# Performance work log

Hardware: AMD Instinct MI355X
Metric: run time of the kernel (lower is better)

Reference implementation:

```python
import jax, jax.numpy as jnp
import numpy as np

D_MODEL = 1024
N_HEAD = 16
HEAD_DIM = D_MODEL // N_HEAD

def setup_inputs() -> dict:
    key = jax.random.key(0)
    k1, k2, k3 = jax.random.split(key, 3)
    x = jax.random.normal(k1, (2, 2048, D_MODEL), dtype=jnp.float32)
    # torch Linear weights: [out_features, in_features]; scale like default init
    w_in = jax.random.normal(k2, (3 * D_MODEL, D_MODEL), dtype=jnp.float32) * (1.0 / np.sqrt(D_MODEL))
    w_out = jax.random.normal(k3, (D_MODEL, D_MODEL), dtype=jnp.float32) * (1.0 / np.sqrt(D_MODEL))
    return {"x": x, "w_in": w_in, "w_out": w_out}

def reference(x, w_in, w_out):
    B, T, D = x.shape
    qkv = jnp.einsum('btd,ed->bte', x, w_in)  # [B,T,3D]
    q, k, v = jnp.split(qkv, 3, axis=2)
    def heads(t):
        return t.reshape(B, T, N_HEAD, HEAD_DIM).transpose(0, 2, 1, 3)  # [B,H,T,hd]
    q, k, v = heads(q), heads(k), heads(v)
    att = jnp.einsum('bhqd,bhkd->bhqk', q, k) / np.sqrt(HEAD_DIM).astype(np.float32)
    # NOTE: original uses .tril() (zeroing, NOT -inf) before softmax — faithful reproduction
    causal = jnp.tril(jnp.ones((T, T), dtype=bool))
    att = jnp.where(causal, att, 0.0)
    att = jax.nn.softmax(att, axis=-1)
    out = jnp.einsum('bhqk,bhkd->bhqd', att, v)
    out = out.transpose(0, 2, 1, 3).reshape(B, T, D)
    return jnp.einsum('btd,ed->bte', out, w_out)
```

## Files before the change

### kernel.cpp

```cpp
#include <hip/hip_runtime.h>
#include <hip/hip_bf16.h>
#include <stdint.h>

#define TSEQ   2048
#define DMODEL 1024
#define NHEAD  16
#define HDIM   64

typedef __attribute__((ext_vector_type(8))) __bf16 bf16x8;
typedef __attribute__((ext_vector_type(4))) float f32x4;
typedef __attribute__((ext_vector_type(8))) unsigned short u16x8;

#define SC_LOG2E 0.18033688011112042f

#if __has_builtin(__builtin_amdgcn_exp2f)
#define EXP2F(x) __builtin_amdgcn_exp2f(x)
#else
#define EXP2F(x) __expf(0.6931471805599453f * (x))
#endif

__device__ __forceinline__ unsigned short f2bf(float f) {
    __hip_bfloat16 h = __float2bfloat16(f);
    return __builtin_bit_cast(unsigned short, h);
}
__device__ __forceinline__ float bf2f(unsigned short u) {
    union { unsigned int i; float f; } v;
    v.i = ((unsigned int)u) << 16;
    return v.f;
}
__device__ __forceinline__ unsigned int cvtpk_bf16(float lo, float hi) {
    unsigned int r;
    asm("v_cvt_pk_bf16_f32 %0, %1, %2" : "=v"(r) : "v"(lo), "v"(hi));
    return r;
}

__device__ __forceinline__ void gld_lds16(const void* g, void* s) {
    __builtin_amdgcn_global_load_lds(
        (__attribute__((address_space(1))) void*)(void*)g,
        (__attribute__((address_space(3))) void*)s, 16, 0, 0);
}

#define NX4  (4096 * 1024 / 4)
#define NWI4 (3072 * 1024 / 4)
#define NWO4 (1024 * 1024 / 4)
__global__ void cast3_kernel(const float* __restrict__ x,
                             const float* __restrict__ wi,
                             const float* __restrict__ wo,
                             unsigned short* __restrict__ ox,
                             unsigned short* __restrict__ owi,
                             unsigned short* __restrict__ owo) {
    int i = blockIdx.x * blockDim.x + threadIdx.x;
    const float* s;
    unsigned short* d;
    int off;
    if (i < NX4)              { s = x;  d = ox;  off = i; }
    else if (i < NX4 + NWI4)  { s = wi; d = owi; off = i - NX4; }
    else                      { s = wo; d = owo; off = i - NX4 - NWI4; }
    float4 v = ((const float4*)s)[off];
    ushort4 u;
    u.x = f2bf(v.x); u.y = f2bf(v.y); u.z = f2bf(v.z); u.w = f2bf(v.w);
    ((ushort4*)d)[off] = u;
}

template<bool STORE_F32>
__global__ __launch_bounds__(256, 3)
void gemm_bt(const unsigned short* __restrict__ A,
             const unsigned short* __restrict__ B,
             void* __restrict__ C, int M, int N, int K) {
    (void)M;
    __shared__ unsigned short As[128 * 32];
    __shared__ unsigned short Bs[128 * 32];
    const int tid = threadIdx.x;
    const int nb = N >> 7;
    const int bm = blockIdx.x / nb;
    const int bn = blockIdx.x % nb;
    const int w  = tid >> 6, l = tid & 63;
    const int wr = w >> 1,  wc = w & 1;
    const int lr = l & 15,  lg = l >> 4;

    f32x4 acc[4][4] = {};

    const unsigned short* Ab = A + (size_t)bm * 128 * K;
    const unsigned short* Bb = B + (size_t)bn * 128 * K;

    const int c0 = tid, c1 = tid + 256;
    const int ar0 = c0 >> 2, ak0 = (c0 & 3) * 8;
    const int ar1 = c1 >> 2, ak1 = (c1 & 3) * 8;

    for (int kt = 0; kt < K; kt += 32) {
        __syncthreads();
        gld_lds16(Ab + (size_t)ar0 * K + kt + ak0, As + c0 * 8);
        gld_lds16(Ab + (size_t)ar1 * K + kt + ak1, As + c1 * 8);
        gld_lds16(Bb + (size_t)ar0 * K + kt + ak0, Bs + c0 * 8);
        gld_lds16(Bb + (size_t)ar1 * K + kt + ak1, Bs + c1 * 8);
        __syncthreads();

        bf16x8 af[4], bfr[4];
#pragma unroll
        for (int i = 0; i < 4; i++)
            af[i] = *(const bf16x8*)(As + (wr * 64 + i * 16 + lr) * 32 + lg * 8);
#pragma unroll
        for (int i = 0; i < 4; i++)
            bfr[i] = *(const bf16x8*)(Bs + (wc * 64 + i * 16 + lr) * 32 + lg * 8);
#pragma unroll
        for (int mi = 0; mi < 4; mi++)
#pragma unroll
            for (int ni = 0; ni < 4; ni++)
                acc[mi][ni] = __builtin_amdgcn_mfma_f32_16x16x32_bf16(
                    af[mi], bfr[ni], acc[mi][ni], 0, 0, 0);
    }

    const int row0 = bm * 128 + wr * 64;
    const int col0 = bn * 128 + wc * 64;
    const float qsc = (!STORE_F32 && bn < 8) ? SC_LOG2E : 1.0f;
#pragma unroll
    for (int mi = 0; mi < 4; mi++)
#pragma unroll
        for (int ni = 0; ni < 4; ni++)
#pragma unroll
            for (int r = 0; r < 4; r++) {
                const int row = row0 + mi * 16 + lg * 4 + r;
                const int col = col0 + ni * 16 + lr;
                if (STORE_F32)
                    ((float*)C)[(size_t)row * N + col] = acc[mi][ni][r];
                else
                    ((unsigned short*)C)[(size_t)row * N + col] =
                        f2bf(acc[mi][ni][r] * qsc);
            }
}

__global__ __launch_bounds__(256)
void vtran_kernel(const unsigned short* __restrict__ qkv,
                  unsigned short* __restrict__ vtg,
                  float* __restrict__ ts) {
    __shared__ unsigned short T[64][72];
    const int bid = blockIdx.x;
    const int kb_ = bid & 31;
    const int bh  = bid >> 5;
    const int b = bh >> 4, h = bh & 15;
    const int tid = threadIdx.x;

    const int r = tid >> 2, cq = (tid & 3) * 16;
    const unsigned short* src =
        qkv + ((size_t)(b * TSEQ + kb_ * 64 + r)) * 3072 + 2048 + h * 64 + cq;
    u16x8 v0 = *(const u16x8*)src;
    u16x8 v1 = *(const u16x8*)(src + 8);
#pragma unroll
    for (int i = 0; i < 8; i++) T[r][cq + i] = v0[i];
#pragma unroll
    for (int i = 0; i < 8; i++) T[r][cq + 8 + i] = v1[i];
    __syncthreads();

    const int d = tid >> 2, kq = (tid & 3) * 16;
    u16x8 o0, o1;
#pragma unroll
    for (int i = 0; i < 8; i++) o0[i] = T[kq + i][d];
#pragma unroll
    for (int i = 0; i < 8; i++) o1[i] = T[kq + 8 + i][d];
    unsigned short* dst = vtg + ((size_t)bh * 64 + d) * TSEQ + kb_ * 64 + kq;
    *(u16x8*)dst = o0;
    *(u16x8*)(dst + 8) = o1;

    float ps = 0.f;
#pragma unroll
    for (int i = 0; i < 8; i++) ps += bf2f(o0[i]) + bf2f(o1[i]);
    ps += __shfl_xor(ps, 1);
    ps += __shfl_xor(ps, 2);
    if ((tid & 3) == 0)
        ts[((size_t)bh * 32 + kb_) * 64 + d] = ps;
}

__global__ __launch_bounds__(256, 2)
void attn_kernel(const unsigned short* __restrict__ qkv,
                 const unsigned short* __restrict__ vtg,
                 const float* __restrict__ ts,
                 unsigned short* __restrict__ out) {
    __shared__ __attribute__((aligned(16))) unsigned short Ks[2][4096];
    __shared__ __attribute__((aligned(16))) unsigned short Vs[2][4096];
    __shared__ __attribute__((aligned(16))) unsigned short Pl[4][32 * 72];

    const int tid = threadIdx.x;
    const int w = tid >> 6, l = tid & 63, lr = l & 15, lg = l >> 4;
    const int bid = blockIdx.x;
    const int j  = bid >> 5;
    const int s  = (j < 8) ? j : 23 - j;
    const int bh = (bid & 7) * 4 + ((bid >> 3) & 3);
    const int b = bh >> 4, h = bh & 15;
    const int strip  = 2 * s + ((w < 2) ? 1 : 0);
    const int lastkt = strip;
    const int ntiles = 2 * s + 2;
    const size_t rowbase = (size_t)b * TSEQ;
    const int qrow0 = strip * 64 + (w & 1) * 32;

    bf16x8 qf[2][2];
#pragma unroll
    for (int mi = 0; mi < 2; mi++) {
        const unsigned short* qp =
            qkv + (rowbase + qrow0 + mi * 16 + lr) * 3072 + h * 64 + lg * 8;
        qf[mi][0] = *(const bf16x8*)qp;
        qf[mi][1] = *(const bf16x8*)(qp + 32);
    }

    const unsigned short* ksrc[2];
    const unsigned short* vsrc[2];
#pragma unroll
    for (int jj = 0; jj < 2; jj++) {
        const int d = tid + jj * 256;
        const int fr = (d >> 7) * 16 + (d & 15);
        const int cc = ((d >> 6) & 1) * 32 + ((d & 63) >> 4) * 8;
        ksrc[jj] = qkv + (rowbase + fr) * 3072 + 1024 + h * 64 + cc;
        vsrc[jj] = vtg + ((size_t)bh * 64 + fr) * TSEQ + cc;
    }

#define STAGE(kt_, bufi) do {                                      \
        const size_t ko_ = (size_t)(kt_) * 64 * 3072;              \
        const int vo_ = (kt_) * 64;                                \
        gld_lds16(ksrc[0] + ko_, &Ks[bufi][tid * 8]);              \
        gld_lds16(ksrc[1] + ko_, &Ks[bufi][tid * 8 + 2048]);       \
        gld_lds16(vsrc[0] + vo_, &Vs[bufi][tid * 8]);              \
        gld_lds16(vsrc[1] + vo_, &Vs[bufi][tid * 8 + 2048]);       \
    } while (0)

    f32x4 o[2][4] = {};
    float ps[2] = {0.f, 0.f};
    unsigned short* pw = &Pl[w][0];

    STAGE(0, 0);
    __syncthreads();

    int cur = 0;
    for (int kt = 0; kt < ntiles; ++kt) {
        if (kt + 1 < ntiles) STAGE(kt + 1, cur ^ 1);

        if (kt <= lastkt) {
            const unsigned short* kc = Ks[cur];
            const unsigned short* vc = Vs[cur];

            bf16x8 kb[4][2];
#pragma unroll
            for (int f = 0; f < 4; f++) {
                kb[f][0] = *(const bf16x8*)(kc + ((f * 2 + 0) * 64 + l) * 8);
                kb[f][1] = *(const bf16x8*)(kc + ((f * 2 + 1) * 64 + l) * 8);
            }

            float pvv[2][4][4];
            __builtin_amdgcn_s_setprio(1);
#pragma unroll
            for (int mi = 0; mi < 2; mi++)
#pragma unroll
                for (int f = 0; f < 4; f++) {
                    f32x4 z = {0.f, 0.f, 0.f, 0.f};
                    f32x4 sv = __builtin_amdgcn_mfma_f32_16x16x32_bf16(kb[f][0], qf[mi][0], z, 0, 0, 0);
                    sv = __builtin_amdgcn_mfma_f32_16x16x32_bf16(kb[f][1], qf[mi][1], sv, 0, 0, 0);
#pragma unroll
                    for (int r = 0; r < 4; r++) pvv[mi][f][r] = sv[r];
                }
            __builtin_amdgcn_s_setprio(0);

            if (kt == lastkt) {
#pragma unroll
                for (int mi = 0; mi < 2; mi++) {
                    const int qr = qrow0 + mi * 16 + lr;
#pragma unroll
                    for (int f = 0; f < 4; f++)
#pragma unroll
                        for (int r = 0; r < 4; r++) {
                            const int kcol = kt * 64 + f * 16 + lg * 4 + r;
                            if (kcol > qr) pvv[mi][f][r] = 0.f;
                        }
                }
            }

#pragma unroll
            for (int mi = 0; mi < 2; mi++)
#pragma unroll
                for (int f = 0; f < 4; f++) {
                    float p0 = EXP2F(pvv[mi][f][0]);
                    float p1 = EXP2F(pvv[mi][f][1]);
                    float p2 = EXP2F(pvv[mi][f][2]);
                    float p3 = EXP2F(pvv[mi][f][3]);
                    ps[mi] += (p0 + p1) + (p2 + p3);
                    uint2 pk;
                    pk.x = cvtpk_bf16(p0, p1);
                    pk.y = cvtpk_bf16(p2, p3);
                    *(uint2*)(pw + (mi * 16 + lr) * 72 + f * 16 + lg * 4) = pk;
                }

            bf16x8 pa[2][2];
#pragma unroll
            for (int mi = 0; mi < 2; mi++) {
                pa[mi][0] = *(const bf16x8*)(pw + (mi * 16 + lr) * 72 + lg * 8);
                pa[mi][1] = *(const bf16x8*)(pw + (mi * 16 + lr) * 72 + 32 + lg * 8);
            }
            bf16x8 vb[4][2];
#pragma unroll
            for (int f2 = 0; f2 < 4; f2++) {
                vb[f2][0] = *(const bf16x8*)(vc + ((f2 * 2 + 0) * 64 + l) * 8);
                vb[f2][1] = *(const bf16x8*)(vc + ((f2 * 2 + 1) * 64 + l) * 8);
            }
            __builtin_amdgcn_s_setprio(1);
#pragma unroll
            for (int mi = 0; mi < 2; mi++)
#pragma unroll
                for (int f2 = 0; f2 < 4; f2++) {
                    o[mi][f2] = __builtin_amdgcn_mfma_f32_16x16x32_bf16(pa[mi][0], vb[f2][0], o[mi][f2], 0, 0, 0);
                    o[mi][f2] = __builtin_amdgcn_mfma_f32_16x16x32_bf16(pa[mi][1], vb[f2][1], o[mi][f2], 0, 0, 0);
                }
            __builtin_amdgcn_s_setprio(0);
        }

        __syncthreads();
        cur ^= 1;
    }
#undef STAGE

#pragma unroll
    for (int mi = 0; mi < 2; mi++) {
        ps[mi] += __shfl_xor(ps[mi], 16);
        ps[mi] += __shfl_xor(ps[mi], 32);
    }
    float rget[2][4];
#pragma unroll
    for (int mi = 0; mi < 2; mi++)
#pragma unroll
        for (int r = 0; r < 4; r++)
            rget[mi][r] = __shfl(ps[mi], lg * 4 + r);

    float tpv[4] = {0.f, 0.f, 0.f, 0.f};
    for (int t = lastkt + 1; t < 32; ++t) {
        const float* tsp = ts + ((size_t)bh * 32 + t) * 64 + lr;
#pragma unroll
        for (int f2 = 0; f2 < 4; f2++) tpv[f2] += tsp[f2 * 16];
    }

    const float nmask = (float)((31 - lastkt) * 64);
#pragma unroll
    for (int mi = 0; mi < 2; mi++)
#pragma unroll
        for (int r = 0; r < 4; r++) {
            const float inv = 1.f / (rget[mi][r] + nmask);
#pragma unroll
            for (int f2 = 0; f2 < 4; f2++) {
                float num = o[mi][f2][r] + tpv[f2];
                out[(rowbase + qrow0 + mi * 16 + lg * 4 + r) * 1024 + h * 64 + f2 * 16 + lr] =
                    f2bf(num * inv);
            }
        }
}

extern "C" void kernel_launch(void* const* d_in, const int* in_sizes, int n_in,
                              void* d_out, int out_size, void* d_ws, size_t ws_size,
                              hipStream_t stream) {
    const float* x     = (const float*)d_in[0];
    const float* w_in  = (const float*)d_in[1];
    const float* w_out = (const float*)d_in[2];

    unsigned short* ws  = (unsigned short*)d_ws;
    unsigned short* xb  = ws;
    unsigned short* wib = xb  + (size_t)4096 * 1024;
    unsigned short* wob = wib + (size_t)3072 * 1024;
    unsigned short* qkv = wob + (size_t)1024 * 1024;
    unsigned short* ao  = qkv + (size_t)4096 * 3072;
    float* tsbuf = (float*)(ao + (size_t)4096 * 1024);
    unsigned short* vtg = (unsigned short*)(tsbuf + 32 * 32 * 64);

    cast3_kernel<<<(NX4 + NWI4 + NWO4) / 256, 256, 0, stream>>>(
        x, w_in, w_out, xb, wib, wob);

    gemm_bt<false><<<(4096 / 128) * (3072 / 128), 256, 0, stream>>>(
        xb, wib, qkv, 4096, 3072, 1024);
    vtran_kernel<<<32 * 32, 256, 0, stream>>>(qkv, vtg, tsbuf);
    attn_kernel<<<512, 256, 0, stream>>>(qkv, vtg, tsbuf, ao);
    gemm_bt<true><<<(4096 / 128) * (1024 / 128), 256, 0, stream>>>(
        ao, wob, (float*)d_out, 4096, 1024, 1024);
}
```

Before: 113.6 us.

## Split attention key tiles across two blocks with atomic accumulation and normalize pass

Each query strip is now handled by two blocks that process alternating (even/odd) key tiles, doubling the grid to 1024 blocks. Partial outputs and row sums are accumulated with float atomics into zeroed buffers, and a new norm kernel divides and casts to bf16. The aim is more parallelism and better load balance in the causal attention. The cost is two memsets, heavy atomic traffic on a 16MB fp32 buffer, and an extra kernel launch. Launch bounds are also raised to three blocks per CU.

Measured after the change: 143.7 us. 1.26x slower.

```diff
diff --git a/kernel.cpp b/kernel.cpp
--- a/kernel.cpp
+++ b/kernel.cpp
@@ -170,11 +170,12 @@
         ts[((size_t)bh * 32 + kb_) * 64 + d] = ps;
 }
 
-__global__ __launch_bounds__(256, 2)
+__global__ __launch_bounds__(256, 3)
 void attn_kernel(const unsigned short* __restrict__ qkv,
                  const unsigned short* __restrict__ vtg,
                  const float* __restrict__ ts,
-                 unsigned short* __restrict__ out) {
+                 float* __restrict__ o_accum,
+                 float* __restrict__ rsum) {
     __shared__ __attribute__((aligned(16))) unsigned short Ks[2][4096];
     __shared__ __attribute__((aligned(16))) unsigned short Vs[2][4096];
     __shared__ __attribute__((aligned(16))) unsigned short Pl[4][32 * 72];
@@ -182,13 +183,15 @@
     const int tid = threadIdx.x;
     const int w = tid >> 6, l = tid & 63, lr = l & 15, lg = l >> 4;
     const int bid = blockIdx.x;
-    const int j  = bid >> 5;
-    const int s  = (j < 8) ? j : 23 - j;
+    const int jj = bid >> 5;
+    const int pairidx = jj >> 1;
+    const int parity  = jj & 1;
+    const int s  = 15 - pairidx;
     const int bh = (bid & 7) * 4 + ((bid >> 3) & 3);
     const int b = bh >> 4, h = bh & 15;
     const int strip  = 2 * s + ((w < 2) ? 1 : 0);
     const int lastkt = strip;
-    const int ntiles = 2 * s + 2;
+    const int ntl = s + 1;
     const size_t rowbase = (size_t)b * TSEQ;
     const int qrow0 = strip * 64 + (w & 1) * 32;
 
@@ -204,12 +207,12 @@
     const unsigned short* ksrc[2];
     const unsigned short* vsrc[2];
 #pragma unroll
-    for (int jj = 0; jj < 2; jj++) {
-        const int d = tid + jj * 256;
+    for (int jx = 0; jx < 2; jx++) {
+        const int d = tid + jx * 256;
         const int fr = (d >> 7) * 16 + (d & 15);
         const int cc = ((d >> 6) & 1) * 32 + ((d & 63) >> 4) * 8;
-        ksrc[jj] = qkv + (rowbase + fr) * 3072 + 1024 + h * 64 + cc;
-        vsrc[jj] = vtg + ((size_t)bh * 64 + fr) * TSEQ + cc;
+        ksrc[jx] = qkv + (rowbase + fr) * 3072 + 1024 + h * 64 + cc;
+        vsrc[jx] = vtg + ((size_t)bh * 64 + fr) * TSEQ + cc;
     }
 
 #define STAGE(kt_, bufi) do {                                      \
@@ -225,16 +228,16 @@
     float ps[2] = {0.f, 0.f};
     unsigned short* pw = &Pl[w][0];
 
-    STAGE(0, 0);
+    STAGE(parity, 0);
     __syncthreads();
 
-    int cur = 0;
-    for (int kt = 0; kt < ntiles; ++kt) {
-        if (kt + 1 < ntiles) STAGE(kt + 1, cur ^ 1);
+    for (int t = 0; t < ntl; ++t) {
+        const int kt = parity + 2 * t;
+        if (t + 1 < ntl) STAGE(parity + 2 * (t + 1), (t + 1) & 1);
 
         if (kt <= lastkt) {
-            const unsigned short* kc = Ks[cur];
-            const unsigned short* vc = Vs[cur];
+            const unsigned short* kc = Ks[t & 1];
+            const unsigned short* vc = Vs[t & 1];
 
             bf16x8 kb[4][2];
 #pragma unroll
@@ -310,7 +313,6 @@
         }
 
         __syncthreads();
-        cur ^= 1;
     }
 #undef STAGE
 
@@ -319,33 +321,48 @@
         ps[mi] += __shfl_xor(ps[mi], 16);
         ps[mi] += __shfl_xor(ps[mi], 32);
     }
-    float rget[2][4];
+    const float nmask = (parity == 0) ? (float)((31 - lastkt) * 64) : 0.f;
+    if (lg == 0) {
+#pragma unroll
+        for (int mi = 0; mi < 2; mi++)
+            atomicAdd(&rsum[(rowbase + qrow0 + mi * 16 + lr) * 16 + h],
+                      ps[mi] + nmask);
+    }
+
+    float tpv[4] = {0.f, 0.f, 0.f, 0.f};
+    if (parity == 0) {
+        for (int t = lastkt + 1; t < 32; ++t) {
+            const float* tsp = ts + ((size_t)bh * 32 + t) * 64 + lr;
+#pragma unroll
+            for (int f2 = 0; f2 < 4; f2++) tpv[f2] += tsp[f2 * 16];
+        }
+    }
+
 #pragma unroll
     for (int mi = 0; mi < 2; mi++)
 #pragma unroll
-        for (int r = 0; r < 4; r++)
-            rget[mi][r] = __shfl(ps[mi], lg * 4 + r);
-
-    float tpv[4] = {0.f, 0.f, 0.f, 0.f};
-    for (int t = lastkt + 1; t < 32; ++t) {
-        const float* tsp = ts + ((size_t)bh * 32 + t) * 64 + lr;
-#pragma unroll
-        for (int f2 = 0; f2 < 4; f2++) tpv[f2] += tsp[f2 * 16];
-    }
-
-    const float nmask = (float)((31 - lastkt) * 64);
-#pragma unroll
-    for (int mi = 0; mi < 2; mi++)
-#pragma unroll
         for (int r = 0; r < 4; r++) {
-            const float inv = 1.f / (rget[mi][r] + nmask);
-#pragma unroll
-            for (int f2 = 0; f2 < 4; f2++) {
-                float num = o[mi][f2][r] + tpv[f2];
-                out[(rowbase + qrow0 + mi * 16 + lg * 4 + r) * 1024 + h * 64 + f2 * 16 + lr] =
-                    f2bf(num * inv);
-            }
+            const size_t row = rowbase + qrow0 + mi * 16 + lg * 4 + r;
+#pragma unroll
+            for (int f2 = 0; f2 < 4; f2++)
+                atomicAdd(&o_accum[row * 1024 + h * 64 + f2 * 16 + lr],
+                          o[mi][f2][r] + tpv[f2]);
         }
+}
+
+__global__ __launch_bounds__(256)
+void norm_kernel(const float* __restrict__ o_accum,
+                 const float* __restrict__ rsum,
+                 unsigned short* __restrict__ ao) {
+    const int i = blockIdx.x * 256 + threadIdx.x;
+    float4 v = ((const float4*)o_accum)[i];
+    const int row = i >> 8;
+    const int h = (i & 255) >> 4;
+    const float inv = 1.f / rsum[row * 16 + h];
+    ushort4 u;
+    u.x = f2bf(v.x * inv); u.y = f2bf(v.y * inv);
+    u.z = f2bf(v.z * inv); u.w = f2bf(v.w * inv);
+    ((ushort4*)ao)[i] = u;
 }
 
 extern "C" void kernel_launch(void* const* d_in, const int* in_sizes, int n_in,
@@ -357,12 +374,14 @@
 
     unsigned short* ws  = (unsigned short*)d_ws;
     unsigned short* xb  = ws;
-    unsigned short* wib = xb  + (size_t)4096 * 1024;
-    unsigned short* wob = wib + (size_t)3072 * 1024;
-    unsigned short* qkv = wob + (size_t)1024 * 1024;
-    unsigned short* ao  = qkv + (size_t)4096 * 3072;
-    float* tsbuf = (float*)(ao + (size_t)4096 * 1024);
-    unsigned short* vtg = (unsigned short*)(tsbuf + 32 * 32 * 64);
+    unsigned short* wib = ws + (size_t)4194304;
+    float* o_accum      = (float*)ws;
+    unsigned short* qkv = ws + (size_t)8388608;
+    unsigned short* ao  = ws + (size_t)20971520;
+    float* tsbuf        = (float*)(ws + (size_t)25165824);
+    unsigned short* vtg = ws + (size_t)25296896;
+    unsigned short* wob = ws + (size_t)29491200;
+    float* rsum         = (float*)(ws + (size_t)30539776);
 
     cast3_kernel<<<(NX4 + NWI4 + NWO4) / 256, 256, 0, stream>>>(
         x, w_in, w_out, xb, wib, wob);
@@ -370,7 +389,13 @@
     gemm_bt<false><<<(4096 / 128) * (3072 / 128), 256, 0, stream>>>(
         xb, wib, qkv, 4096, 3072, 1024);
     vtran_kernel<<<32 * 32, 256, 0, stream>>>(qkv, vtg, tsbuf);
-    attn_kernel<<<512, 256, 0, stream>>>(qkv, vtg, tsbuf, ao);
+
+    hipMemsetAsync(o_accum, 0, (size_t)4096 * 1024 * 4, stream);
+    hipMemsetAsync(rsum, 0, (size_t)4096 * 16 * 4, stream);
+
+    attn_kernel<<<1024, 256, 0, stream>>>(qkv, vtg, tsbuf, o_accum, rsum);
+    norm_kernel<<<4096, 256, 0, stream>>>(o_accum, rsum, ao);
+
     gemm_bt<true><<<(4096 / 128) * (1024 / 128), 256, 0, stream>>>(
         ao, wob, (float*)d_out, 4096, 1024, 1024);
 }
```

## Fuse V transpose and key-block column sums into QKV GEMM epilogue

Applied to the files above, without the earlier changes.

The QKV projection GEMM now writes the V tiles straight into the transposed per-head layout and computes the 64-row column sums in its epilogue. This replaces the separate vtran kernel. It removes one kernel launch and a full extra read and write of the V portion of qkv. In exchange, the epilogue does strided 8-byte stores across the transposed layout. The sums are now taken from fp32 accumulators rather than bf16-rounded values, which changes rounding slightly.

After: 108.7 us. 1.05x faster.

```diff
diff --git a/kernel.cpp b/kernel.cpp
--- a/kernel.cpp
+++ b/kernel.cpp
@@ -62,11 +62,13 @@
     ((ushort4*)d)[off] = u;
 }
 
-template<bool STORE_F32>
+template<int MODE>
 __global__ __launch_bounds__(256, 3)
 void gemm_bt(const unsigned short* __restrict__ A,
              const unsigned short* __restrict__ B,
-             void* __restrict__ C, int M, int N, int K) {
+             void* __restrict__ C, int M, int N, int K,
+             unsigned short* __restrict__ vtg,
+             float* __restrict__ ts) {
     (void)M;
     __shared__ unsigned short As[128 * 32];
     __shared__ unsigned short Bs[128 * 32];
@@ -112,7 +114,41 @@
 
     const int row0 = bm * 128 + wr * 64;
     const int col0 = bn * 128 + wc * 64;
-    const float qsc = (!STORE_F32 && bn < 8) ? SC_LOG2E : 1.0f;
+
+    if (MODE == 0 && bn >= 16) {
+        const int h     = (bn - 16) * 2 + wc;
+        const int krow0 = row0;
+        const int bb    = krow0 >> 11;
+        const int kloc0 = krow0 & 2047;
+        const int bh    = bb * 16 + h;
+        const int t     = kloc0 >> 6;
+#pragma unroll
+        for (int ni = 0; ni < 4; ni++) {
+            const size_t dbase = ((size_t)(bh * 64 + ni * 16 + lr)) * TSEQ;
+#pragma unroll
+            for (int mi = 0; mi < 4; mi++) {
+                uint2 pk;
+                pk.x = cvtpk_bf16(acc[mi][ni][0], acc[mi][ni][1]);
+                pk.y = cvtpk_bf16(acc[mi][ni][2], acc[mi][ni][3]);
+                *(uint2*)(vtg + dbase + kloc0 + mi * 16 + lg * 4) = pk;
+            }
+        }
+#pragma unroll
+        for (int ni = 0; ni < 4; ni++) {
+            float sum = 0.f;
+#pragma unroll
+            for (int mi = 0; mi < 4; mi++)
+#pragma unroll
+                for (int r = 0; r < 4; r++) sum += acc[mi][ni][r];
+            sum += __shfl_xor(sum, 16);
+            sum += __shfl_xor(sum, 32);
+            if (lg == 0)
+                ts[((size_t)bh * 32 + t) * 64 + ni * 16 + lr] = sum;
+        }
+        return;
+    }
+
+    const float qsc = (MODE == 0 && bn < 8) ? SC_LOG2E : 1.0f;
 #pragma unroll
     for (int mi = 0; mi < 4; mi++)
 #pragma unroll
@@ -121,53 +157,12 @@
             for (int r = 0; r < 4; r++) {
                 const int row = row0 + mi * 16 + lg * 4 + r;
                 const int col = col0 + ni * 16 + lr;
-                if (STORE_F32)
+                if (MODE == 1)
                     ((float*)C)[(size_t)row * N + col] = acc[mi][ni][r];
                 else
                     ((unsigned short*)C)[(size_t)row * N + col] =
                         f2bf(acc[mi][ni][r] * qsc);
             }
-}
-
-__global__ __launch_bounds__(256)
-void vtran_kernel(const unsigned short* __restrict__ qkv,
-                  unsigned short* __restrict__ vtg,
-                  float* __restrict__ ts) {
-    __shared__ unsigned short T[64][72];
-    const int bid = blockIdx.x;
-    const int kb_ = bid & 31;
-    const int bh  = bid >> 5;
-    const int b = bh >> 4, h = bh & 15;
-    const int tid = threadIdx.x;
-
-    const int r = tid >> 2, cq = (tid & 3) * 16;
-    const unsigned short* src =
-        qkv + ((size_t)(b * TSEQ + kb_ * 64 + r)) * 3072 + 2048 + h * 64 + cq;
-    u16x8 v0 = *(const u16x8*)src;
-    u16x8 v1 = *(const u16x8*)(src + 8);
-#pragma unroll
-    for (int i = 0; i < 8; i++) T[r][cq + i] = v0[i];
-#pragma unroll
-    for (int i = 0; i < 8; i++) T[r][cq + 8 + i] = v1[i];
-    __syncthreads();
-
-    const int d = tid >> 2, kq = (tid & 3) * 16;
-    u16x8 o0, o1;
-#pragma unroll
-    for (int i = 0; i < 8; i++) o0[i] = T[kq + i][d];
-#pragma unroll
-    for (int i = 0; i < 8; i++) o1[i] = T[kq + 8 + i][d];
-    unsigned short* dst = vtg + ((size_t)bh * 64 + d) * TSEQ + kb_ * 64 + kq;
-    *(u16x8*)dst = o0;
-    *(u16x8*)(dst + 8) = o1;
-
-    float ps = 0.f;
-#pragma unroll
-    for (int i = 0; i < 8; i++) ps += bf2f(o0[i]) + bf2f(o1[i]);
-    ps += __shfl_xor(ps, 1);
-    ps += __shfl_xor(ps, 2);
-    if ((tid & 3) == 0)
-        ts[((size_t)bh * 32 + kb_) * 64 + d] = ps;
 }
 
 __global__ __launch_bounds__(256, 2)
@@ -367,10 +362,9 @@
     cast3_kernel<<<(NX4 + NWI4 + NWO4) / 256, 256, 0, stream>>>(
         x, w_in, w_out, xb, wib, wob);
 
-    gemm_bt<false><<<(4096 / 128) * (3072 / 128), 256, 0, stream>>>(
-        xb, wib, qkv, 4096, 3072, 1024);
-    vtran_kernel<<<32 * 32, 256, 0, stream>>>(qkv, vtg, tsbuf);
+    gemm_bt<0><<<(4096 / 128) * (3072 / 128), 256, 0, stream>>>(
+        xb, wib, qkv, 4096, 3072, 1024, vtg, tsbuf);
     attn_kernel<<<512, 256, 0, stream>>>(qkv, vtg, tsbuf, ao);
-    gemm_bt<true><<<(4096 / 128) * (1024 / 128), 256, 0, stream>>>(
-        ao, wob, (float*)d_out, 4096, 1024, 1024);
-}
+    gemm_bt<1><<<(4096 / 128) * (1024 / 128), 256, 0, stream>>>(
+        ao, wob, (float*)d_out, 4096, 1024, 1024, nullptr, nullptr);
+}
```
